# Optimization experiments

Hardware: AMD Instinct MI355X
Metric: run time of the kernel (lower is better)

Reference implementation:

```python
import jax, jax.numpy as jnp
import numpy as np

B, S, D, H, P = 4, 512, 512, 8, 16
DK = D // H  # 64


def setup_inputs() -> dict:
    k0 = jax.random.key(0)
    ks = jax.random.split(k0, 10)
    std = 0.02
    lin = lambda k, shape: jax.random.normal(k, shape, dtype=jnp.float32) * std
    inp = {}
    inp["query"] = jax.random.normal(ks[0], (B, S, D), dtype=jnp.float32)
    inp["key"] = jax.random.normal(ks[1], (B, S, D), dtype=jnp.float32)
    inp["value"] = jax.random.normal(ks[2], (B, S, D), dtype=jnp.float32)
    inp["Wq"] = lin(ks[3], (D, D)); inp["bq"] = jnp.zeros((D,), jnp.float32)
    inp["Wk"] = lin(ks[4], (D, D)); inp["bk"] = jnp.zeros((D,), jnp.float32)
    inp["Wv"] = lin(ks[5], (D, D)); inp["bv"] = jnp.zeros((D,), jnp.float32)
    inp["Wo"] = lin(ks[6], (D, D)); inp["bo"] = jnp.zeros((D,), jnp.float32)
    inp["rel_table"] = lin(ks[7], (2 * P + 1, DK))  # nn.Embedding(2P+1, d_k)
    inp["gamma"] = jnp.ones((D,), jnp.float32)
    inp["beta"] = jnp.zeros((D,), jnp.float32)
    inp["mask"] = jnp.ones((B, S), dtype=jnp.int32)
    inp["relative_positions"] = jax.random.randint(ks[8], (B, S, S, DK), -32, 33, dtype=jnp.int32)
    return inp


def reference(query, key, value, Wq, bq, Wk, bk, Wv, bv, Wo, bo, rel_table, gamma, beta, mask, relative_positions):
    b, s, d = query.shape
    dk = rel_table.shape[1]
    h = d // dk
    pmax = (rel_table.shape[0] - 1) // 2

    def heads(x, W, bias):
        return (x @ W.T + bias).reshape(b, s, h, dk).transpose(0, 2, 1, 3)  # [b,h,s,dk]

    Q = heads(query, Wq, bq)
    K = heads(key, Wk, bk)
    V = heads(value, Wv, bv)

    scores = jnp.einsum('bhid,bhjd->bhij', Q, K) / jnp.sqrt(jnp.float32(dk))

    # torch: einsum('bhid,bijde->bhije', Q, emb(idx)).mean(-1)
    # mean over e commutes with the d-contraction -> pre-average the table.
    idx = jnp.clip(relative_positions, -pmax, pmax) + pmax  # [b,i,j,d]
    bias_d = rel_table.mean(axis=-1)[idx]                   # [b,i,j,d]
    scores = scores + jnp.einsum('bhid,bijd->bhij', Q, bias_d)

    scores = jnp.where(mask[:, None, None, :] == 0, jnp.float32(-1e9), scores)
    attn = jax.nn.softmax(scores, axis=-1)  # dropout is identity in eval

    ctx = jnp.einsum('bhij,bhjd->bhid', attn, V).transpose(0, 2, 1, 3).reshape(b, s, d)
    out = ctx @ Wo.T + bo

    x = out + query  # residual
    mu = x.mean(-1, keepdims=True)
    var = x.var(-1, keepdims=True)
    y = (x - mu) / jnp.sqrt(var + 1e-5) * gamma + beta
    return (y, attn)
```

## Files before the change

kernel.cpp:

```cpp
#include <hip/hip_runtime.h>
#include <hip/hip_bf16.h>

#define BB 4
#define SS 512
#define DD 512
#define HH 8
#define DK 64
#define PP 16
#define TSZ 33

typedef __bf16 bf16x8 __attribute__((ext_vector_type(8)));
typedef __bf16 bf16x4 __attribute__((ext_vector_type(4)));
typedef float  f32x4  __attribute__((ext_vector_type(4)));

union U8 { bf16x8 v; int u[4]; };

__device__ inline bf16x8 cvt8(const float* __restrict__ p) {
    f32x4 a = *(const f32x4*)p;
    f32x4 b = *(const f32x4*)(p + 4);
    bf16x8 r;
    r[0] = (__bf16)a[0]; r[1] = (__bf16)a[1]; r[2] = (__bf16)a[2]; r[3] = (__bf16)a[3];
    r[4] = (__bf16)b[0]; r[5] = (__bf16)b[1]; r[6] = (__bf16)b[2]; r[7] = (__bf16)b[3];
    return r;
}

__global__ void prep_kernel(const float* __restrict__ rel_table, float* __restrict__ Tm,
                            const float* __restrict__ Wo, __bf16* __restrict__ Wobf) {
    int b = blockIdx.x, t = threadIdx.x;
    if (b == 0) {
        if (t < TSZ) {
            float s = 0.f;
            for (int e = 0; e < DK; ++e) s += rel_table[t * DK + e];
            Tm[t] = s * (1.f / DK);
        }
    } else {
        int idx = ((b - 1) * 256 + t) * 8;
        *(bf16x8*)(Wobf + idx) = cvt8(Wo + idx);
    }
}

__global__ void proj_mfma_kernel(const float* __restrict__ X0, const float* __restrict__ X1,
                                 const float* __restrict__ X2,
                                 const float* __restrict__ W0, const float* __restrict__ W1,
                                 const float* __restrict__ W2,
                                 const float* __restrict__ B0, const float* __restrict__ B1,
                                 const float* __restrict__ B2,
                                 __bf16* __restrict__ O0, __bf16* __restrict__ O1,
                                 __bf16* __restrict__ O2) {
    int z = blockIdx.z;
    const float* X = (z == 0) ? X0 : (z == 1) ? X1 : X2;
    const float* W = (z == 0) ? W0 : (z == 1) ? W1 : W2;
    const float* bias = (z == 0) ? B0 : (z == 1) ? B1 : B2;
    __bf16* out = (z == 0) ? O0 : (z == 1) ? O1 : O2;
    int mode = (z == 2);

    int lane = threadIdx.x, wave = threadIdx.y;
    int tm = blockIdx.y * 4 + wave;
    int tn = blockIdx.x;
    int m = lane & 15, quad = lane >> 4;

    const float* arow = X + (size_t)(tm * 16 + m) * DD + quad * 8;
    const float* brow = W + (size_t)(tn * 16 + m) * DD + quad * 8;

    f32x4 acc = {0.f, 0.f, 0.f, 0.f};
    for (int k0 = 0; k0 < DD; k0 += 32) {
        bf16x8 a = cvt8(arow + k0);
        bf16x8 b = cvt8(brow + k0);
        acc = __builtin_amdgcn_mfma_f32_16x16x32_bf16(a, b, acc, 0, 0, 0);
    }

    int col = tn * 16 + m;
    int h = col >> 6, dk = col & (DK - 1);
    float bv = bias[col];
#pragma unroll
    for (int r = 0; r < 4; ++r) {
        int rowg = tm * 16 + quad * 4 + r;
        int b = rowg >> 9, i = rowg & (SS - 1);
        float v = acc[r] + bv;
        if (mode == 0)
            out[((size_t)(b * HH + h) * SS + i) * DK + dk] = (__bf16)v;
        else
            out[((size_t)(b * HH + h) * DK + dk) * SS + i] = (__bf16)v;
    }
}

__launch_bounds__(512, 4)
__global__ void f1_kernel(const __bf16* __restrict__ Qbf, const __bf16* __restrict__ Kbf,
                          const int* __restrict__ relpos, const float* __restrict__ Tm,
                          const int* __restrict__ mask, __bf16* __restrict__ pws,
                          float* __restrict__ pm, float* __restrict__ pl) {
    __shared__ float bias_sh[8 * 16 * 132];

    int l = threadIdx.x, w = threadIdx.y;
    int jq = blockIdx.x, i0 = blockIdx.y, b = blockIdx.z;
    int m = l & 15, quad = l >> 4;

    float tmf = Tm[l < TSZ ? l : 0];
    int tmb = (int)__builtin_bit_cast(unsigned short, (__bf16)tmf);

    {
        const int ISTR = SS * DK;
        const int* rbase = relpos + ((size_t)(b * SS + i0 * 16) * SS + jq * 128 + w * 16 + m) * DK + quad * 8;
        int4 u0 = *(const int4*)(rbase);
        int4 u1 = *(const int4*)(rbase + 4);
        int4 u2 = *(const int4*)(rbase + 32);
        int4 u3 = *(const int4*)(rbase + 36);
        const int* pb1 = rbase + ISTR;
        int4 v0 = *(const int4*)(pb1);
        int4 v1 = *(const int4*)(pb1 + 4);
        int4 v2 = *(const int4*)(pb1 + 32);
        int4 v3 = *(const int4*)(pb1 + 36);
        for (int i = 0; i < 16; ++i) {
            int4 n0, n1, n2, n3;
            if (i < 14) {
                const int* nb = rbase + (i + 2) * ISTR;
                n0 = *(const int4*)(nb);
                n1 = *(const int4*)(nb + 4);
                n2 = *(const int4*)(nb + 32);
                n3 = *(const int4*)(nb + 36);
            }
            const __bf16* qp = Qbf + ((size_t)(b * HH + (m & 7)) * SS + i0 * 16 + i) * DK + quad * 8;
            bf16x8 A0 = *(const bf16x8*)qp;
            bf16x8 A1 = *(const bf16x8*)(qp + 32);
#define LUT(vv) __builtin_amdgcn_ds_bpermute((min(max((vv), -PP), PP) + PP) << 2, tmb)
            U8 Bf0, Bf1;
            Bf0.u[0] = LUT(u0.x) | (LUT(u0.y) << 16);
            Bf0.u[1] = LUT(u0.z) | (LUT(u0.w) << 16);
            Bf0.u[2] = LUT(u1.x) | (LUT(u1.y) << 16);
            Bf0.u[3] = LUT(u1.z) | (LUT(u1.w) << 16);
            Bf1.u[0] = LUT(u2.x) | (LUT(u2.y) << 16);
            Bf1.u[1] = LUT(u2.z) | (LUT(u2.w) << 16);
            Bf1.u[2] = LUT(u3.x) | (LUT(u3.y) << 16);
            Bf1.u[3] = LUT(u3.z) | (LUT(u3.w) << 16);
#undef LUT
            f32x4 accB = {0.f, 0.f, 0.f, 0.f};
            accB = __builtin_amdgcn_mfma_f32_16x16x32_bf16(A0, Bf0.v, accB, 0, 0, 0);
            accB = __builtin_amdgcn_mfma_f32_16x16x32_bf16(A1, Bf1.v, accB, 0, 0, 0);
            if (quad < 2) {
#pragma unroll
                for (int r = 0; r < 4; ++r) {
                    int h = quad * 4 + r;
                    bias_sh[h * 2112 + i * 132 + w * 16 + m] = accB[r];
                }
            }
            u0 = v0; u1 = v1; u2 = v2; u3 = v3;
            v0 = n0; v1 = n1; v2 = n2; v3 = n3;
        }
    }

    const __bf16* qrow = Qbf + ((size_t)(b * HH + w) * SS + i0 * 16 + m) * DK + quad * 8;
    bf16x8 a0 = *(const bf16x8*)qrow;
    bf16x8 a1 = *(const bf16x8*)(qrow + 32);

    f32x4 acc[8];
#pragma unroll
    for (int jt = 0; jt < 8; ++jt) {
        const __bf16* krow = Kbf + ((size_t)(b * HH + w) * SS + jq * 128 + jt * 16 + m) * DK + quad * 8;
        bf16x8 b0 = *(const bf16x8*)krow;
        bf16x8 b1 = *(const bf16x8*)(krow + 32);
        f32x4 c = {0.f, 0.f, 0.f, 0.f};
        c = __builtin_amdgcn_mfma_f32_16x16x32_bf16(a0, b0, c, 0, 0, 0);
        c = __builtin_amdgcn_mfma_f32_16x16x32_bf16(a1, b1, c, 0, 0, 0);
        acc[jt] = c;
    }

    __syncthreads();

#pragma unroll
    for (int jt = 0; jt < 8; ++jt) {
#pragma unroll
        for (int r = 0; r < 4; ++r) {
            float bv = bias_sh[w * 2112 + (quad * 4 + r) * 132 + jt * 16 + m];
            acc[jt][r] = acc[jt][r] * 0.125f + bv;
        }
    }

#pragma unroll
    for (int jt = 0; jt < 8; ++jt) {
        int mv = mask[b * SS + jq * 128 + jt * 16 + m];
        if (mv == 0) {
#pragma unroll
            for (int r = 0; r < 4; ++r) acc[jt][r] = -1e9f;
        }
    }

#pragma unroll
    for (int r = 0; r < 4; ++r) {
        float mx = -1e30f;
#pragma unroll
        for (int jt = 0; jt < 8; ++jt) mx = fmaxf(mx, acc[jt][r]);
        mx = fmaxf(mx, __shfl_xor(mx, 1));
        mx = fmaxf(mx, __shfl_xor(mx, 2));
        mx = fmaxf(mx, __shfl_xor(mx, 4));
        mx = fmaxf(mx, __shfl_xor(mx, 8));
        float sum = 0.f;
#pragma unroll
        for (int jt = 0; jt < 8; ++jt) {
            float e = __expf(acc[jt][r] - mx);
            acc[jt][r] = e;
            sum += e;
        }
        sum += __shfl_xor(sum, 1);
        sum += __shfl_xor(sum, 2);
        sum += __shfl_xor(sum, 4);
        sum += __shfl_xor(sum, 8);
        if (m == 0) {
            int row = i0 * 16 + quad * 4 + r;
            pm[((size_t)(b * HH + w) * SS + row) * 4 + jq] = mx;
            pl[((size_t)(b * HH + w) * SS + row) * 4 + jq] = sum;
        }
    }

#pragma unroll
    for (int jt = 0; jt < 8; ++jt) {
#pragma unroll
        for (int r = 0; r < 4; ++r) {
            pws[((size_t)(b * HH + w) * SS + i0 * 16 + quad * 4 + r) * SS
                + jq * 128 + jt * 16 + m] = (__bf16)acc[jt][r];
        }
    }
}

__launch_bounds__(256, 4)
__global__ void f2_kernel(const __bf16* __restrict__ pws, const float* __restrict__ pm,
                          const float* __restrict__ pl, const __bf16* __restrict__ Vt,
                          float* __restrict__ attn, __bf16* __restrict__ ctx_bsd) {
    __shared__ float scl[4][16];

    int t = threadIdx.x;
    int l = t & 63, wv = t >> 6;
    int i0 = blockIdx.x, bh = blockIdx.y;

    if (t < 16) {
        int row = i0 * 16 + t;
        f32x4 m4 = *(const f32x4*)(pm + ((size_t)bh * SS + row) * 4);
        f32x4 l4 = *(const f32x4*)(pl + ((size_t)bh * SS + row) * 4);
        float M = fmaxf(fmaxf(m4[0], m4[1]), fmaxf(m4[2], m4[3]));
        float e0 = __expf(m4[0] - M), e1 = __expf(m4[1] - M);
        float e2 = __expf(m4[2] - M), e3 = __expf(m4[3] - M);
        float L = l4[0] * e0 + l4[1] * e1 + l4[2] * e2 + l4[3] * e3;
        float inv = 1.f / L;
        scl[0][t] = e0 * inv; scl[1][t] = e1 * inv;
        scl[2][t] = e2 * inv; scl[3][t] = e3 * inv;
    }
    __syncthreads();

    const __bf16* pbase = pws + ((size_t)bh * SS + i0 * 16) * SS;
    float* abase = attn + ((size_t)bh * SS + i0 * 16) * SS;

    int colq = l >> 4;
#pragma unroll
    for (int rr = 0; rr < 4; ++rr) {
        int row = wv * 4 + rr;
        bf16x8 p = *(const bf16x8*)(pbase + (size_t)row * SS + l * 8);
        float s = scl[colq][row];
        f32x4 o0, o1;
        o0[0] = (float)p[0] * s; o0[1] = (float)p[1] * s;
        o0[2] = (float)p[2] * s; o0[3] = (float)p[3] * s;
        o1[0] = (float)p[4] * s; o1[1] = (float)p[5] * s;
        o1[2] = (float)p[6] * s; o1[3] = (float)p[7] * s;
        __builtin_nontemporal_store(o0, (f32x4*)(abase + (size_t)row * SS + l * 8));
        __builtin_nontemporal_store(o1, (f32x4*)(abase + (size_t)row * SS + l * 8 + 4));
    }

    int m = l & 15, quad = l >> 4;
    const __bf16* prow = pbase + (size_t)m * SS + quad * 8;
    const __bf16* vrow = Vt + ((size_t)bh * DK + wv * 16 + m) * SS + quad * 8;
    float ctxv[4] = {0.f, 0.f, 0.f, 0.f};
#pragma unroll
    for (int q = 0; q < 4; ++q) {
        f32x4 acc = {0.f, 0.f, 0.f, 0.f};
#pragma unroll
        for (int kk = 0; kk < 4; ++kk) {
            int k0 = q * 128 + kk * 32;
            bf16x8 aF = *(const bf16x8*)(prow + k0);
            bf16x8 bF = *(const bf16x8*)(vrow + k0);
            acc = __builtin_amdgcn_mfma_f32_16x16x32_bf16(aF, bF, acc, 0, 0, 0);
        }
#pragma unroll
        for (int r = 0; r < 4; ++r) ctxv[r] += acc[r] * scl[q][quad * 4 + r];
    }
    int b = bh >> 3, h = bh & 7;
#pragma unroll
    for (int r = 0; r < 4; ++r) {
        ctx_bsd[((size_t)(b * SS + i0 * 16 + quad * 4 + r)) * DD + h * DK + wv * 16 + m]
            = (__bf16)ctxv[r];
    }
}

__launch_bounds__(512, 2)
__global__ void outln_kernel(const __bf16* __restrict__ Xc, const __bf16* __restrict__ Wobf,
                             const float* __restrict__ bo, const float* __restrict__ query,
                             const float* __restrict__ gamma, const float* __restrict__ beta,
                             float* __restrict__ y) {
    __shared__ float xsh[16 * 516];

    int lane = threadIdx.x, w = threadIdx.y;
    int tm = blockIdx.x;
    int m = lane & 15, quad = lane >> 4;

    const __bf16* arow = Xc + (size_t)(tm * 16 + m) * DD + quad * 8;

    f32x4 acc[4] = {{0.f,0.f,0.f,0.f},{0.f,0.f,0.f,0.f},{0.f,0.f,0.f,0.f},{0.f,0.f,0.f,0.f}};
    for (int k0 = 0; k0 < DD; k0 += 32) {
        bf16x8 a = *(const bf16x8*)(arow + k0);
#pragma unroll
        for (int tile = 0; tile < 4; ++tile) {
            const __bf16* brow = Wobf + (size_t)(w * 64 + tile * 16 + m) * DD + k0 + quad * 8;
            bf16x8 b = *(const bf16x8*)brow;
            acc[tile] = __builtin_amdgcn_mfma_f32_16x16x32_bf16(a, b, acc[tile], 0, 0, 0);
        }
    }

#pragma unroll
    for (int tile = 0; tile < 4; ++tile) {
        int col = w * 64 + tile * 16 + m;
        float bv = bo[col];
#pragma unroll
        for (int r = 0; r < 4; ++r) {
            int row = quad * 4 + r;
            int rowg = tm * 16 + row;
            xsh[row * 516 + col] = acc[tile][r] + bv + query[(size_t)rowg * DD + col];
        }
    }
    __syncthreads();

#pragma unroll
    for (int rr = 0; rr < 2; ++rr) {
        int row = w * 2 + rr;
        const float* xr = &xsh[row * 516];
        f32x4 xa = *(const f32x4*)(xr + lane * 8);
        f32x4 xb = *(const f32x4*)(xr + lane * 8 + 4);
        float s  = xa[0] + xa[1] + xa[2] + xa[3] + xb[0] + xb[1] + xb[2] + xb[3];
        float sq = xa[0]*xa[0] + xa[1]*xa[1] + xa[2]*xa[2] + xa[3]*xa[3]
                 + xb[0]*xb[0] + xb[1]*xb[1] + xb[2]*xb[2] + xb[3]*xb[3];
#pragma unroll
        for (int off = 32; off >= 1; off >>= 1) {
            s  += __shfl_xor(s, off);
            sq += __shfl_xor(sq, off);
        }
        float mu = s * (1.f / DD);
        float var = sq * (1.f / DD) - mu * mu;
        float inv = rsqrtf(var + 1e-5f);
        f32x4 g0 = *(const f32x4*)(gamma + lane * 8);
        f32x4 g1 = *(const f32x4*)(gamma + lane * 8 + 4);
        f32x4 b0 = *(const f32x4*)(beta + lane * 8);
        f32x4 b1 = *(const f32x4*)(beta + lane * 8 + 4);
        f32x4 o0, o1;
#pragma unroll
        for (int e = 0; e < 4; ++e) {
            o0[e] = (xa[e] - mu) * inv * g0[e] + b0[e];
            o1[e] = (xb[e] - mu) * inv * g1[e] + b1[e];
        }
        float* yr = y + (size_t)(tm * 16 + row) * DD + lane * 8;
        *(f32x4*)yr = o0;
        *(f32x4*)(yr + 4) = o1;
    }
}

extern "C" void kernel_launch(void* const* d_in, const int* in_sizes, int n_in,
                              void* d_out, int out_size, void* d_ws, size_t ws_size,
                              hipStream_t stream) {
    const float* query  = (const float*)d_in[0];
    const float* key    = (const float*)d_in[1];
    const float* value  = (const float*)d_in[2];
    const float* Wq     = (const float*)d_in[3];
    const float* bq     = (const float*)d_in[4];
    const float* Wk     = (const float*)d_in[5];
    const float* bk     = (const float*)d_in[6];
    const float* Wv     = (const float*)d_in[7];
    const float* bv     = (const float*)d_in[8];
    const float* Wo     = (const float*)d_in[9];
    const float* bo     = (const float*)d_in[10];
    const float* rtab   = (const float*)d_in[11];
    const float* gamma  = (const float*)d_in[12];
    const float* beta   = (const float*)d_in[13];
    const int*   mask   = (const int*)d_in[14];
    const int*   relpos = (const int*)d_in[15];

    float* out = (float*)d_out;
    float* y    = out;
    float* attn = out + (size_t)BB * SS * DD;

    char* wsb = (char*)d_ws;
    float*  Tm    = (float*)wsb;   wsb += 256;
    __bf16* Qbf   = (__bf16*)wsb;  wsb += (size_t)BB * HH * SS * DK * 2;
    __bf16* Kbf   = (__bf16*)wsb;  wsb += (size_t)BB * HH * SS * DK * 2;
    __bf16* Vtbf  = (__bf16*)wsb;  wsb += (size_t)BB * HH * DK * SS * 2;
    __bf16* ctxbf = (__bf16*)wsb;  wsb += (size_t)BB * SS * DD * 2;
    __bf16* Wobf  = (__bf16*)wsb;  wsb += (size_t)DD * DD * 2;
    __bf16* pws   = (__bf16*)wsb;  wsb += (size_t)BB * HH * SS * SS * 2;
    float*  pm    = (float*)wsb;   wsb += (size_t)BB * HH * SS * 4 * 4;
    float*  pl    = (float*)wsb;   wsb += (size_t)BB * HH * SS * 4 * 4;

    hipLaunchKernelGGL(prep_kernel, dim3(1 + (DD * DD) / (256 * 8)), dim3(256), 0, stream,
                       rtab, Tm, Wo, Wobf);

    dim3 wblk(64, 4);
    hipLaunchKernelGGL(proj_mfma_kernel, dim3(DD / 16, (BB * SS) / 64, 3), wblk, 0, stream,
                       query, key, value, Wq, Wk, Wv, bq, bk, bv, Qbf, Kbf, Vtbf);

    hipLaunchKernelGGL(f1_kernel, dim3(4, SS / 16, BB), dim3(64, 8), 0, stream,
                       Qbf, Kbf, relpos, Tm, mask, pws, pm, pl);

    hipLaunchKernelGGL(f2_kernel, dim3(SS / 16, BB * HH), dim3(256), 0, stream,
                       pws, pm, pl, Vtbf, attn, ctxbf);

    hipLaunchKernelGGL(outln_kernel, dim3((BB * SS) / 16), dim3(64, 8), 0, stream,
                       ctxbf, Wobf, bo, query, gamma, beta, y);
}
```

Baseline: 539.8 us.

## Pre-convert inputs and weights to bf16, widen projection tiles, nontemporal relpos loads

The prep kernel now converts Wq/Wk/Wv/Wo and the query/key/value activations to bf16 up front. The projection kernel reads bf16 directly and computes four 16-column tiles per wave, reusing each A fragment across them. The f1 kernel loads relative_positions with nontemporal hints so the large streaming read does not pollute the cache. Together these aim to cut repeated fp32 loads and conversions in the GEMM, at the cost of an extra pass writing and reading bf16 copies of the activations.

```diff
diff --git a/kernel.cpp b/kernel.cpp
--- a/kernel.cpp
+++ b/kernel.cpp
@@ -12,6 +12,7 @@
 typedef __bf16 bf16x8 __attribute__((ext_vector_type(8)));
 typedef __bf16 bf16x4 __attribute__((ext_vector_type(4)));
 typedef float  f32x4  __attribute__((ext_vector_type(4)));
+typedef int    i32x4  __attribute__((ext_vector_type(4)));
 
 union U8 { bf16x8 v; int u[4]; };
 
@@ -25,62 +26,83 @@
 }
 
 __global__ void prep_kernel(const float* __restrict__ rel_table, float* __restrict__ Tm,
-                            const float* __restrict__ Wo, __bf16* __restrict__ Wobf) {
-    int b = blockIdx.x, t = threadIdx.x;
-    if (b == 0) {
+                            const float* __restrict__ Wq, const float* __restrict__ Wk,
+                            const float* __restrict__ Wv, const float* __restrict__ Wo,
+                            const float* __restrict__ q, const float* __restrict__ k,
+                            const float* __restrict__ v,
+                            __bf16* __restrict__ Wqb, __bf16* __restrict__ Wkb,
+                            __bf16* __restrict__ Wvb, __bf16* __restrict__ Wob,
+                            __bf16* __restrict__ qb, __bf16* __restrict__ kb,
+                            __bf16* __restrict__ vb) {
+    int bid = blockIdx.x, t = threadIdx.x;
+    if (bid == 0) {
         if (t < TSZ) {
             float s = 0.f;
             for (int e = 0; e < DK; ++e) s += rel_table[t * DK + e];
             Tm[t] = s * (1.f / DK);
         }
-    } else {
-        int idx = ((b - 1) * 256 + t) * 8;
-        *(bf16x8*)(Wobf + idx) = cvt8(Wo + idx);
-    }
-}
-
-__global__ void proj_mfma_kernel(const float* __restrict__ X0, const float* __restrict__ X1,
-                                 const float* __restrict__ X2,
-                                 const float* __restrict__ W0, const float* __restrict__ W1,
-                                 const float* __restrict__ W2,
+        return;
+    }
+    int idx = (bid - 1) * 256 + t;
+    const float* s; __bf16* d; int off;
+    if (idx < 131072) {
+        int w = idx >> 15; off = idx & 32767;
+        s = (w == 0) ? Wq : (w == 1) ? Wk : (w == 2) ? Wv : Wo;
+        d = (w == 0) ? Wqb : (w == 1) ? Wkb : (w == 2) ? Wvb : Wob;
+    } else if (idx < 262144) { s = q; d = qb; off = idx - 131072; }
+    else if (idx < 393216)   { s = k; d = kb; off = idx - 262144; }
+    else                     { s = v; d = vb; off = idx - 393216; }
+    *(bf16x8*)(d + (size_t)off * 8) = cvt8(s + (size_t)off * 8);
+}
+
+__global__ void proj_mfma_kernel(const __bf16* __restrict__ X0, const __bf16* __restrict__ X1,
+                                 const __bf16* __restrict__ X2,
+                                 const __bf16* __restrict__ W0, const __bf16* __restrict__ W1,
+                                 const __bf16* __restrict__ W2,
                                  const float* __restrict__ B0, const float* __restrict__ B1,
                                  const float* __restrict__ B2,
                                  __bf16* __restrict__ O0, __bf16* __restrict__ O1,
                                  __bf16* __restrict__ O2) {
     int z = blockIdx.z;
-    const float* X = (z == 0) ? X0 : (z == 1) ? X1 : X2;
-    const float* W = (z == 0) ? W0 : (z == 1) ? W1 : W2;
+    const __bf16* X = (z == 0) ? X0 : (z == 1) ? X1 : X2;
+    const __bf16* W = (z == 0) ? W0 : (z == 1) ? W1 : W2;
     const float* bias = (z == 0) ? B0 : (z == 1) ? B1 : B2;
     __bf16* out = (z == 0) ? O0 : (z == 1) ? O1 : O2;
     int mode = (z == 2);
 
     int lane = threadIdx.x, wave = threadIdx.y;
     int tm = blockIdx.y * 4 + wave;
-    int tn = blockIdx.x;
+    int tn0 = blockIdx.x * 4;
     int m = lane & 15, quad = lane >> 4;
 
-    const float* arow = X + (size_t)(tm * 16 + m) * DD + quad * 8;
-    const float* brow = W + (size_t)(tn * 16 + m) * DD + quad * 8;
-
-    f32x4 acc = {0.f, 0.f, 0.f, 0.f};
+    const __bf16* arow = X + (size_t)(tm * 16 + m) * DD + quad * 8;
+
+    f32x4 acc[4] = {{0.f,0.f,0.f,0.f},{0.f,0.f,0.f,0.f},{0.f,0.f,0.f,0.f},{0.f,0.f,0.f,0.f}};
     for (int k0 = 0; k0 < DD; k0 += 32) {
-        bf16x8 a = cvt8(arow + k0);
-        bf16x8 b = cvt8(brow + k0);
-        acc = __builtin_amdgcn_mfma_f32_16x16x32_bf16(a, b, acc, 0, 0, 0);
-    }
-
-    int col = tn * 16 + m;
-    int h = col >> 6, dk = col & (DK - 1);
-    float bv = bias[col];
-#pragma unroll
-    for (int r = 0; r < 4; ++r) {
-        int rowg = tm * 16 + quad * 4 + r;
-        int b = rowg >> 9, i = rowg & (SS - 1);
-        float v = acc[r] + bv;
-        if (mode == 0)
-            out[((size_t)(b * HH + h) * SS + i) * DK + dk] = (__bf16)v;
-        else
-            out[((size_t)(b * HH + h) * DK + dk) * SS + i] = (__bf16)v;
+        bf16x8 a = *(const bf16x8*)(arow + k0);
+#pragma unroll
+        for (int tt = 0; tt < 4; ++tt) {
+            const __bf16* brow = W + (size_t)((tn0 + tt) * 16 + m) * DD + k0 + quad * 8;
+            bf16x8 b = *(const bf16x8*)brow;
+            acc[tt] = __builtin_amdgcn_mfma_f32_16x16x32_bf16(a, b, acc[tt], 0, 0, 0);
+        }
+    }
+
+#pragma unroll
+    for (int tt = 0; tt < 4; ++tt) {
+        int col = (tn0 + tt) * 16 + m;
+        int h = col >> 6, dk = col & (DK - 1);
+        float bv = bias[col];
+#pragma unroll
+        for (int r = 0; r < 4; ++r) {
+            int rowg = tm * 16 + quad * 4 + r;
+            int b = rowg >> 9, i = rowg & (SS - 1);
+            float vv = acc[tt][r] + bv;
+            if (mode == 0)
+                out[((size_t)(b * HH + h) * SS + i) * DK + dk] = (__bf16)vv;
+            else
+                out[((size_t)(b * HH + h) * DK + dk) * SS + i] = (__bf16)vv;
+        }
     }
 }
 
@@ -101,37 +123,37 @@
     {
         const int ISTR = SS * DK;
         const int* rbase = relpos + ((size_t)(b * SS + i0 * 16) * SS + jq * 128 + w * 16 + m) * DK + quad * 8;
-        int4 u0 = *(const int4*)(rbase);
-        int4 u1 = *(const int4*)(rbase + 4);
-        int4 u2 = *(const int4*)(rbase + 32);
-        int4 u3 = *(const int4*)(rbase + 36);
+        i32x4 u0 = __builtin_nontemporal_load((const i32x4*)(rbase));
+        i32x4 u1 = __builtin_nontemporal_load((const i32x4*)(rbase + 4));
+        i32x4 u2 = __builtin_nontemporal_load((const i32x4*)(rbase + 32));
+        i32x4 u3 = __builtin_nontemporal_load((const i32x4*)(rbase + 36));
         const int* pb1 = rbase + ISTR;
-        int4 v0 = *(const int4*)(pb1);
-        int4 v1 = *(const int4*)(pb1 + 4);
-        int4 v2 = *(const int4*)(pb1 + 32);
-        int4 v3 = *(const int4*)(pb1 + 36);
+        i32x4 v0 = __builtin_nontemporal_load((const i32x4*)(pb1));
+        i32x4 v1 = __builtin_nontemporal_load((const i32x4*)(pb1 + 4));
+        i32x4 v2 = __builtin_nontemporal_load((const i32x4*)(pb1 + 32));
+        i32x4 v3 = __builtin_nontemporal_load((const i32x4*)(pb1 + 36));
         for (int i = 0; i < 16; ++i) {
-            int4 n0, n1, n2, n3;
+            i32x4 n0, n1, n2, n3;
             if (i < 14) {
                 const int* nb = rbase + (i + 2) * ISTR;
-                n0 = *(const int4*)(nb);
-                n1 = *(const int4*)(nb + 4);
-                n2 = *(const int4*)(nb + 32);
-                n3 = *(const int4*)(nb + 36);
+                n0 = __builtin_nontemporal_load((const i32x4*)(nb));
+                n1 = __builtin_nontemporal_load((const i32x4*)(nb + 4));
+                n2 = __builtin_nontemporal_load((const i32x4*)(nb + 32));
+                n3 = __builtin_nontemporal_load((const i32x4*)(nb + 36));
             }
             const __bf16* qp = Qbf + ((size_t)(b * HH + (m & 7)) * SS + i0 * 16 + i) * DK + quad * 8;
             bf16x8 A0 = *(const bf16x8*)qp;
             bf16x8 A1 = *(const bf16x8*)(qp + 32);
 #define LUT(vv) __builtin_amdgcn_ds_bpermute((min(max((vv), -PP), PP) + PP) << 2, tmb)
             U8 Bf0, Bf1;
-            Bf0.u[0] = LUT(u0.x) | (LUT(u0.y) << 16);
-            Bf0.u[1] = LUT(u0.z) | (LUT(u0.w) << 16);
-            Bf0.u[2] = LUT(u1.x) | (LUT(u1.y) << 16);
-            Bf0.u[3] = LUT(u1.z) | (LUT(u1.w) << 16);
-            Bf1.u[0] = LUT(u2.x) | (LUT(u2.y) << 16);
-            Bf1.u[1] = LUT(u2.z) | (LUT(u2.w) << 16);
-            Bf1.u[2] = LUT(u3.x) | (LUT(u3.y) << 16);
-            Bf1.u[3] = LUT(u3.z) | (LUT(u3.w) << 16);
+            Bf0.u[0] = LUT(u0[0]) | (LUT(u0[1]) << 16);
+            Bf0.u[1] = LUT(u0[2]) | (LUT(u0[3]) << 16);
+            Bf0.u[2] = LUT(u1[0]) | (LUT(u1[1]) << 16);
+            Bf0.u[3] = LUT(u1[2]) | (LUT(u1[3]) << 16);
+            Bf1.u[0] = LUT(u2[0]) | (LUT(u2[1]) << 16);
+            Bf1.u[1] = LUT(u2[2]) | (LUT(u2[3]) << 16);
+            Bf1.u[2] = LUT(u3[0]) | (LUT(u3[1]) << 16);
+            Bf1.u[3] = LUT(u3[2]) | (LUT(u3[3]) << 16);
 #undef LUT
             f32x4 accB = {0.f, 0.f, 0.f, 0.f};
             accB = __builtin_amdgcn_mfma_f32_16x16x32_bf16(A0, Bf0.v, accB, 0, 0, 0);
@@ -388,17 +410,23 @@
     __bf16* Kbf   = (__bf16*)wsb;  wsb += (size_t)BB * HH * SS * DK * 2;
     __bf16* Vtbf  = (__bf16*)wsb;  wsb += (size_t)BB * HH * DK * SS * 2;
     __bf16* ctxbf = (__bf16*)wsb;  wsb += (size_t)BB * SS * DD * 2;
-    __bf16* Wobf  = (__bf16*)wsb;  wsb += (size_t)DD * DD * 2;
+    __bf16* Wqb   = (__bf16*)wsb;  wsb += (size_t)DD * DD * 2;
+    __bf16* Wkb   = (__bf16*)wsb;  wsb += (size_t)DD * DD * 2;
+    __bf16* Wvb   = (__bf16*)wsb;  wsb += (size_t)DD * DD * 2;
+    __bf16* Wob   = (__bf16*)wsb;  wsb += (size_t)DD * DD * 2;
+    __bf16* qb    = (__bf16*)wsb;  wsb += (size_t)BB * SS * DD * 2;
+    __bf16* kb    = (__bf16*)wsb;  wsb += (size_t)BB * SS * DD * 2;
+    __bf16* vb    = (__bf16*)wsb;  wsb += (size_t)BB * SS * DD * 2;
     __bf16* pws   = (__bf16*)wsb;  wsb += (size_t)BB * HH * SS * SS * 2;
     float*  pm    = (float*)wsb;   wsb += (size_t)BB * HH * SS * 4 * 4;
     float*  pl    = (float*)wsb;   wsb += (size_t)BB * HH * SS * 4 * 4;
 
-    hipLaunchKernelGGL(prep_kernel, dim3(1 + (DD * DD) / (256 * 8)), dim3(256), 0, stream,
-                       rtab, Tm, Wo, Wobf);
-
-    dim3 wblk(64, 4);
-    hipLaunchKernelGGL(proj_mfma_kernel, dim3(DD / 16, (BB * SS) / 64, 3), wblk, 0, stream,
-                       query, key, value, Wq, Wk, Wv, bq, bk, bv, Qbf, Kbf, Vtbf);
+    hipLaunchKernelGGL(prep_kernel, dim3(2049), dim3(256), 0, stream,
+                       rtab, Tm, Wq, Wk, Wv, Wo, query, key, value,
+                       Wqb, Wkb, Wvb, Wob, qb, kb, vb);
+
+    hipLaunchKernelGGL(proj_mfma_kernel, dim3(DD / 64, (BB * SS) / 64, 3), dim3(64, 4), 0, stream,
+                       qb, kb, vb, Wqb, Wkb, Wvb, bq, bk, bv, Qbf, Kbf, Vtbf);
 
     hipLaunchKernelGGL(f1_kernel, dim3(4, SS / 16, BB), dim3(64, 8), 0, stream,
                        Qbf, Kbf, relpos, Tm, mask, pws, pm, pl);
@@ -407,5 +435,5 @@
                        pws, pm, pl, Vtbf, attn, ctxbf);
 
     hipLaunchKernelGGL(outln_kernel, dim3((BB * SS) / 16), dim3(64, 8), 0, stream,
-                       ctxbf, Wobf, bo, query, gamma, beta, y);
-}
+                       ctxbf, Wob, bo, query, gamma, beta, y);
+}
```

Result: faster. 473.2 us (-12.3%).
